# Performance work log

Hardware: AMD Instinct MI355X
Metric: run time of the kernel (lower is better)

Reference implementation:

```python
import jax, jax.numpy as jnp
import numpy as np

N = 50000
E = 1000000
D_IN = 128
D_HID = 128
D_EMB = 128
D_DEG = 32
NEG_SLOPE = 0.2


def _add_self_loops(src, dst, n):
    loop = jnp.arange(n, dtype=src.dtype)
    return jnp.concatenate([src, loop]), jnp.concatenate([dst, loop])


def gat_conv(x, src, dst, W, a_src, a_dst, b, n):
    """PyG GATConv, heads=1, add_self_loops=True. src/dst already include self loops."""
    h = x @ W                                   # [n, d_out]
    hs = h[src]                                 # [e, d_out] gather (message sources)
    e = jax.nn.leaky_relu(hs @ a_src + h[dst] @ a_dst, NEG_SLOPE)  # [e]
    m = jax.ops.segment_max(e, dst, num_segments=n)
    e = jnp.exp(e - m[dst])
    denom = jax.ops.segment_sum(e, dst, num_segments=n)
    alpha = e / (denom[dst] + 1e-16)
    out = jax.ops.segment_sum(alpha[:, None] * hs, dst, num_segments=n)
    return out + b


def setup_inputs() -> dict:
    key = jax.random.key(0)
    ks = jax.random.split(key, 24)
    p = lambda k, shape: (jax.random.normal(k, shape, dtype=jnp.float32) * 0.05)
    inp = {
        "x_o": jax.random.normal(ks[0], (N, D_IN), dtype=jnp.float32),
        "degree_o": jax.random.normal(ks[1], (N, D_DEG), dtype=jnp.float32),
        "edge_index_o": jax.random.randint(ks[2], (2, E), 0, N, dtype=jnp.int32),
        "edge_index_s": jax.random.randint(ks[3], (2, E), 0, N, dtype=jnp.int32),
        # GAT layer params: o1, o2, s1, s2
        "W_o1": p(ks[4], (D_IN, D_HID)), "a_src_o1": p(ks[5], (D_HID,)), "a_dst_o1": p(ks[6], (D_HID,)), "b_o1": jnp.zeros((D_HID,), jnp.float32),
        "W_o2": p(ks[7], (D_HID, D_EMB)), "a_src_o2": p(ks[8], (D_EMB,)), "a_dst_o2": p(ks[9], (D_EMB,)), "b_o2": jnp.zeros((D_EMB,), jnp.float32),
        "W_s1": p(ks[10], (D_IN, D_HID)), "a_src_s1": p(ks[11], (D_HID,)), "a_dst_s1": p(ks[12], (D_HID,)), "b_s1": jnp.zeros((D_HID,), jnp.float32),
        "W_s2": p(ks[13], (D_HID, D_EMB)), "a_src_s2": p(ks[14], (D_EMB,)), "a_dst_s2": p(ks[15], (D_EMB,)), "b_s2": jnp.zeros((D_EMB,), jnp.float32),
        "W_pred": p(ks[16], (2 * D_EMB + D_DEG, 2)), "b_pred": jnp.zeros((2,), jnp.float32),
    }
    return inp


def reference(x_o, degree_o,
              W_o1, a_src_o1, a_dst_o1, b_o1,
              W_o2, a_src_o2, a_dst_o2, b_o2,
              W_s1, a_src_s1, a_dst_s1, b_s1,
              W_s2, a_src_s2, a_dst_s2, b_s2,
              W_pred, b_pred,
              edge_index_o, edge_index_s):
    n = x_o.shape[0]
    src_o, dst_o = _add_self_loops(edge_index_o[0], edge_index_o[1], n)
    src_s, dst_s = _add_self_loops(edge_index_s[0], edge_index_s[1], n)

    # branch o (original graph); dropout is identity in eval mode
    x1_o = jax.nn.relu(gat_conv(x_o, src_o, dst_o, W_o1, a_src_o1, a_dst_o1, b_o1, n))
    x2_o = gat_conv(x1_o, src_o, dst_o, W_o2, a_src_o2, a_dst_o2, b_o2, n)
    # branch s (second graph)
    x1_s = jax.nn.relu(gat_conv(x_o, src_s, dst_s, W_s1, a_src_s1, a_dst_s1, b_s1, n))
    x2_s = gat_conv(x1_s, src_s, dst_s, W_s2, a_src_s2, a_dst_s2, b_s2, n)

    x2_os = jnp.concatenate([x2_o, x2_s, degree_o], axis=1)   # [n, 2*emb+deg]
    attn = jax.nn.softmax(x2_os @ W_pred + b_pred, axis=1)    # [n, 2]
    pred = attn[:, :1] * x2_o + attn[:, 1:] * x2_s            # [n, emb]
    return pred
```

## Files before the change

### kernel.cpp

```cpp
#include <hip/hip_runtime.h>
#include <hip/hip_fp16.h>
#include <math.h>


#define LRELU(v) ((v) > 0.f ? (v) : 0.2f * (v))

#define BSHIFT 7
#define BSIZE  128
#define MAXB   512
#define CHUNK  4096
#define EPT    16
#define MAXE   4352
#define CAPI   (MAXE + BSIZE)
#define WTSZ   17408

typedef _Float16 half8 __attribute__((ext_vector_type(8)));
typedef float f32x4 __attribute__((ext_vector_type(4)));


__global__ __launch_bounds__(256) void k_bin_scatter(
    const int* __restrict__ src_o, const int* __restrict__ dst_o,
    const int* __restrict__ src_s, const int* __restrict__ dst_s,
    int* bcur_o, int* bcur_s, int* ebin_o, int* ebin_s, int E)
{
    __shared__ int cnt[MAXB];
    __shared__ int gb[MAXB];
    int t = threadIdx.x;
    int base = blockIdx.x * CHUNK;

    for (int g = 0; g < 2; g++) {
        const int* srcp = g ? src_s : src_o;
        const int* dstp = g ? dst_s : dst_o;
        int* bcur = g ? bcur_s : bcur_o;
        int* ebin = g ? ebin_s : ebin_o;
        for (int i = t; i < MAXB; i += 256) cnt[i] = 0;
        __syncthreads();
        int pk[EPT], bk[EPT], rk[EPT];
        #pragma unroll
        for (int j = 0; j < EPT; j++) {
            int e = base + j * 256 + t;
            bk[j] = -1; pk[j] = 0; rk[j] = 0;
            if (e < E) {
                int d = dstp[e];
                int s = srcp[e];
                int bb = d >> BSHIFT;
                bk[j] = bb;
                pk[j] = ((d & (BSIZE - 1)) << 16) | s;
                rk[j] = atomicAdd(&cnt[bb], 1);
            }
        }
        __syncthreads();
        for (int i = t; i < MAXB; i += 256) {
            int c = cnt[i];
            gb[i] = c ? atomicAdd(&bcur[i], c) : 0;
        }
        __syncthreads();
        #pragma unroll
        for (int j = 0; j < EPT; j++) {
            if (bk[j] >= 0) {
                int p = gb[bk[j]] + rk[j];
                if (p < (bk[j] + 1) * MAXE) ebin[p] = pk[j];
            }
        }
        __syncthreads();
    }
}


__global__ __launch_bounds__(256) void k_prepw(
    const float* __restrict__ W0, const float* __restrict__ W1,
    const float* __restrict__ W2, const float* __restrict__ W3,
    _Float16* __restrict__ WtG, int* bcur_o, int* bcur_s, int nbuck)
{
    int i = blockIdx.x * 256 + threadIdx.x;
    if (i < nbuck) { bcur_o[i] = i * MAXE; bcur_s[i] = i * MAXE; }
    int w = i >> 14;
    int rem = i & 16383;
    int nn = rem >> 7;
    int k = rem & 127;
    const float* W = (w == 0) ? W0 : (w == 1) ? W1 : (w == 2) ? W2 : W3;
    WtG[w * WTSZ + nn * 136 + k] = (_Float16)W[k * 128 + nn];
}


__device__ __forceinline__ void sd_epilogue(
    const f32x4* acc, const float* a_src, const float* a_dst,
    float* Svec, float* Dvec, int m0, int wave, int lane, int m, int q, int n)
{
    float sp[4] = {0.f, 0.f, 0.f, 0.f};
    float dp[4] = {0.f, 0.f, 0.f, 0.f};
    #pragma unroll
    for (int nt = 0; nt < 8; nt++) {
        float asv = a_src[nt * 16 + m];
        float adv = a_dst[nt * 16 + m];
        #pragma unroll
        for (int r = 0; r < 4; r++) {
            sp[r] = fmaf(acc[nt][r], asv, sp[r]);
            dp[r] = fmaf(acc[nt][r], adv, dp[r]);
        }
    }
    #pragma unroll
    for (int msk = 1; msk < 16; msk <<= 1) {
        #pragma unroll
        for (int r = 0; r < 4; r++) {
            sp[r] += __shfl_xor(sp[r], msk);
            dp[r] += __shfl_xor(dp[r], msk);
        }
    }
    if (m == 0) {
        #pragma unroll
        for (int r = 0; r < 4; r++) {
            int row = m0 + wave * 16 + q * 4 + r;
            if (row < n) { Svec[row] = sp[r]; Dvec[row] = dp[r]; }
        }
    }
}

__device__ __forceinline__ void d_to_lds(
    _Float16* As, const f32x4* acc, int wave, int m, int q)
{
    #pragma unroll
    for (int nt = 0; nt < 8; nt++) {
        #pragma unroll
        for (int r = 0; r < 4; r++) {
            As[(wave * 16 + q * 4 + r) * 136 + nt * 16 + m] = (_Float16)acc[nt][r];
        }
    }
}

__device__ __forceinline__ void lds_to_h(
    const _Float16* As, __half* H, int m0, int tid, int n)
{
    for (int i = tid; i < 1024; i += 256) {
        int r = i >> 4;
        int c8 = (i & 15) << 3;
        int row = m0 + r;
        if (row < n)
            *(uint4*)&H[(size_t)row * 128 + c8] = *(const uint4*)&As[r * 136 + c8];
    }
}


__device__ __forceinline__ void sort_body(
    char* SMEM, int b,
    const int* __restrict__ ebin, const int* __restrict__ bcur,
    int* __restrict__ off, int* __restrict__ dend,
    unsigned short* __restrict__ idx, int N)
{
    int* pack   = (int*)SMEM;
    int* sorted = pack + MAXE;
    int* cnt4   = sorted + MAXE + BSIZE;
    int* s2     = cnt4 + 4 * (BSIZE + 1);
    int* noff   = s2 + (BSIZE + 1);

    int t = threadIdx.x;
    int wave = t >> 6;
    int node0 = b << BSHIFT;
    int nloc = min(BSIZE, N - node0);
    int ebeg = b * MAXE;
    int ne = min(bcur[b] - ebeg, MAXE);
    int ib = b * CAPI;

    for (int i = t; i < ne; i += 256) pack[i] = ebin[ebeg + i];
    for (int i = t; i < 4 * (BSIZE + 1); i += 256) cnt4[i] = 0;
    __syncthreads();
    for (int i = t; i < ne; i += 256)
        atomicAdd(&cnt4[wave * (BSIZE + 1) + (pack[i] >> 16)], 1);
    __syncthreads();
    int c0 = 0, c1 = 0, c2 = 0, c3 = 0, selfc = 0;
    if (t < BSIZE + 1) {
        c0 = cnt4[0 * (BSIZE + 1) + t];
        c1 = cnt4[1 * (BSIZE + 1) + t];
        c2 = cnt4[2 * (BSIZE + 1) + t];
        c3 = cnt4[3 * (BSIZE + 1) + t];
        selfc = (t < nloc) ? 1 : 0;
        s2[t] = c0 + c1 + c2 + c3 + selfc;
    }
    __syncthreads();
    for (int d = 1; d <= BSIZE; d <<= 1) {
        int v = (t < BSIZE + 1 && t >= d) ? s2[t - d] : 0;
        __syncthreads();
        if (t < BSIZE + 1) s2[t] += v;
        __syncthreads();
    }
    if (t < BSIZE + 1) noff[t] = s2[t] - (c0 + c1 + c2 + c3 + selfc);
    __syncthreads();
    if (t < nloc) {
        int base0 = noff[t] + 1;
        cnt4[0 * (BSIZE + 1) + t] = base0;
        cnt4[1 * (BSIZE + 1) + t] = base0 + c0;
        cnt4[2 * (BSIZE + 1) + t] = base0 + c0 + c1;
        cnt4[3 * (BSIZE + 1) + t] = base0 + c0 + c1 + c2;
        sorted[noff[t]] = node0 + t;
        off[node0 + t]  = ib + noff[t];
        dend[node0 + t] = ib + s2[t];
    }
    __syncthreads();
    for (int i = t; i < ne; i += 256) {
        int p = atomicAdd(&cnt4[wave * (BSIZE + 1) + (pack[i] >> 16)], 1);
        sorted[p] = pack[i] & 0xffff;
    }
    __syncthreads();
    int tot = ne + nloc;
    for (int i = t; i < tot; i += 256) idx[ib + i] = (unsigned short)sorted[i];
}


__device__ __forceinline__ void gemm1_body(
    char* SMEM, int m0,
    const float* __restrict__ X,
    const _Float16* __restrict__ WtO, const _Float16* __restrict__ WtS,
    const float* __restrict__ asO, const float* __restrict__ adO,
    const float* __restrict__ asS, const float* __restrict__ adS,
    __half* __restrict__ HO, __half* __restrict__ HS,
    float* __restrict__ SO, float* __restrict__ DO,
    float* __restrict__ SS, float* __restrict__ DS, int n)
{
    _Float16* As = (_Float16*)SMEM;
    _Float16* Wt = As + 64 * 136;
    int tid = threadIdx.x;

    for (int i = tid; i < WTSZ / 8; i += 256)
        ((uint4*)Wt)[i] = ((const uint4*)WtO)[i];
    for (int i = tid; i < 64 * 32; i += 256) {
        int r = i >> 5;
        int c4 = (i & 31) << 2;
        int row = m0 + r; if (row >= n) row = n - 1;
        float4 v = *(const float4*)&X[(size_t)row * 128 + c4];
        _Float16* p = &As[r * 136 + c4];
        p[0] = (_Float16)v.x; p[1] = (_Float16)v.y;
        p[2] = (_Float16)v.z; p[3] = (_Float16)v.w;
    }
    __syncthreads();

    int wave = tid >> 6;
    int lane = tid & 63;
    int m = lane & 15;
    int q = lane >> 4;
    int arow = wave * 16 + m;

    f32x4 accO[8], accS[8];
    #pragma unroll
    for (int nt = 0; nt < 8; nt++) accO[nt] = (f32x4){0.f, 0.f, 0.f, 0.f};
    #pragma unroll
    for (int k0 = 0; k0 < 128; k0 += 32) {
        half8 a = *(half8*)&As[arow * 136 + k0 + q * 8];
        #pragma unroll
        for (int nt = 0; nt < 8; nt++) {
            half8 b = *(half8*)&Wt[(nt * 16 + m) * 136 + k0 + q * 8];
            accO[nt] = __builtin_amdgcn_mfma_f32_16x16x32_f16(a, b, accO[nt], 0, 0, 0);
        }
    }
    sd_epilogue(accO, asO, adO, SO, DO, m0, wave, lane, m, q, n);
    __syncthreads();
    for (int i = tid; i < WTSZ / 8; i += 256)
        ((uint4*)Wt)[i] = ((const uint4*)WtS)[i];
    __syncthreads();
    #pragma unroll
    for (int nt = 0; nt < 8; nt++) accS[nt] = (f32x4){0.f, 0.f, 0.f, 0.f};
    #pragma unroll
    for (int k0 = 0; k0 < 128; k0 += 32) {
        half8 a = *(half8*)&As[arow * 136 + k0 + q * 8];
        #pragma unroll
        for (int nt = 0; nt < 8; nt++) {
            half8 b = *(half8*)&Wt[(nt * 16 + m) * 136 + k0 + q * 8];
            accS[nt] = __builtin_amdgcn_mfma_f32_16x16x32_f16(a, b, accS[nt], 0, 0, 0);
        }
    }
    sd_epilogue(accS, asS, adS, SS, DS, m0, wave, lane, m, q, n);

    __syncthreads();
    d_to_lds(As, accO, wave, m, q);
    __syncthreads();
    lds_to_h(As, HO, m0, tid, n);
    __syncthreads();
    d_to_lds(As, accS, wave, m, q);
    __syncthreads();
    lds_to_h(As, HS, m0, tid, n);
}


__global__ __launch_bounds__(256) void k_sortgemm1(
    const int* __restrict__ ebin_o, const int* __restrict__ bcur_o,
    int* __restrict__ off_o, int* __restrict__ dend_o, unsigned short* __restrict__ idx_o,
    const int* __restrict__ ebin_s, const int* __restrict__ bcur_s,
    int* __restrict__ off_s, int* __restrict__ dend_s, unsigned short* __restrict__ idx_s,
    const float* __restrict__ X,
    const _Float16* __restrict__ WtO, const _Float16* __restrict__ WtS,
    const float* __restrict__ asO, const float* __restrict__ adO,
    const float* __restrict__ asS, const float* __restrict__ adS,
    __half* __restrict__ HO, __half* __restrict__ HS,
    float* __restrict__ SO, float* __restrict__ DO,
    float* __restrict__ SS, float* __restrict__ DS,
    int N, int nbuck)
{
    __shared__ __align__(16) char SMEM[52224];
    int bid = blockIdx.x;
    if (bid < 2 * nbuck) {
        if (bid < nbuck)
            sort_body(SMEM, bid, ebin_o, bcur_o, off_o, dend_o, idx_o, N);
        else
            sort_body(SMEM, bid - nbuck, ebin_s, bcur_s, off_s, dend_s, idx_s, N);
    } else {
        gemm1_body(SMEM, (bid - 2 * nbuck) * 64, X, WtO, WtS,
                   asO, adO, asS, adS, HO, HS, SO, DO, SS, DS, N);
    }
}


__global__ __launch_bounds__(256) void k_gemm2(
    const __half* __restrict__ X0, const __half* __restrict__ X1,
    const _Float16* __restrict__ WtA, const _Float16* __restrict__ WtB,
    const float* __restrict__ as0, const float* __restrict__ ad0,
    const float* __restrict__ as1, const float* __restrict__ ad1,
    __half* __restrict__ H0, __half* __restrict__ H1,
    float* __restrict__ S0, float* __restrict__ D0,
    float* __restrict__ S1, float* __restrict__ D1,
    int n)
{
    int br = blockIdx.y;
    const __half* X = br ? X1 : X0;
    const _Float16* WtGp = br ? WtB : WtA;
    const float* a_src = br ? as1 : as0;
    const float* a_dst = br ? ad1 : ad0;
    __half* H = br ? H1 : H0;
    float* Svec = br ? S1 : S0;
    float* Dvec = br ? D1 : D0;

    __shared__ _Float16 As[64 * 136];
    __shared__ _Float16 Wt[128 * 136];
    int tid = threadIdx.x;
    int m0 = blockIdx.x * 64;

    for (int i = tid; i < WTSZ / 8; i += 256)
        ((uint4*)Wt)[i] = ((const uint4*)WtGp)[i];
    for (int i = tid; i < 64 * 16; i += 256) {
        int r = i >> 4;
        int c8 = (i & 15) << 3;
        int row = m0 + r; if (row >= n) row = n - 1;
        *(uint4*)&As[r * 136 + c8] = *(const uint4*)&X[(size_t)row * 128 + c8];
    }
    __syncthreads();

    int wave = tid >> 6;
    int lane = tid & 63;
    int m = lane & 15;
    int q = lane >> 4;
    int arow = wave * 16 + m;

    f32x4 acc[8];
    #pragma unroll
    for (int nt = 0; nt < 8; nt++) acc[nt] = (f32x4){0.f, 0.f, 0.f, 0.f};
    #pragma unroll
    for (int k0 = 0; k0 < 128; k0 += 32) {
        half8 a = *(half8*)&As[arow * 136 + k0 + q * 8];
        #pragma unroll
        for (int nt = 0; nt < 8; nt++) {
            half8 b = *(half8*)&Wt[(nt * 16 + m) * 136 + k0 + q * 8];
            acc[nt] = __builtin_amdgcn_mfma_f32_16x16x32_f16(a, b, acc[nt], 0, 0, 0);
        }
    }
    sd_epilogue(acc, a_src, a_dst, Svec, Dvec, m0, wave, lane, m, q, n);
    __syncthreads();
    d_to_lds(As, acc, wave, m, q);
    __syncthreads();
    lds_to_h(As, H, m0, tid, n);
}


__device__ __forceinline__ void agg_core(
    const __half* __restrict__ H, const float* __restrict__ Svec, float dn,
    const unsigned short* __restrict__ idx, int beg, int end,
    int lane, int q, int subl, float* acc, float& denom)
{
    #pragma unroll
    for (int j = 0; j < 8; j++) acc[j] = 0.f;
    denom = 0.f;
    for (int base = beg; base < end; base += 64) {
        int cnt = min(64, end - base);
        float w = 0.f;
        int s = 0;
        if (lane < cnt) {
            s = idx[base + lane];
            w = __expf(LRELU(Svec[s] + dn));
        }
        denom += w;
        int cnt16 = (cnt + 15) & ~15;
        for (int kk = 0; kk < cnt16; kk += 16) {
            int k0 = kk + q;
            float w0 = __shfl(w, k0);
            float w1 = __shfl(w, k0 + 4);
            float w2 = __shfl(w, k0 + 8);
            float w3 = __shfl(w, k0 + 12);
            int s0 = __shfl(s, k0);
            int s1 = __shfl(s, k0 + 4);
            int s2 = __shfl(s, k0 + 8);
            int s3 = __shfl(s, k0 + 12);
            uint4 u0 = ((const uint4*)(H + (size_t)s0 * 128))[subl];
            uint4 u1 = ((const uint4*)(H + (size_t)s1 * 128))[subl];
            uint4 u2 = ((const uint4*)(H + (size_t)s2 * 128))[subl];
            uint4 u3 = ((const uint4*)(H + (size_t)s3 * 128))[subl];
            const _Float16* p;
            p = (const _Float16*)&u0;
            #pragma unroll
            for (int j = 0; j < 8; j++) acc[j] = fmaf((float)p[j], w0, acc[j]);
            p = (const _Float16*)&u1;
            #pragma unroll
            for (int j = 0; j < 8; j++) acc[j] = fmaf((float)p[j], w1, acc[j]);
            p = (const _Float16*)&u2;
            #pragma unroll
            for (int j = 0; j < 8; j++) acc[j] = fmaf((float)p[j], w2, acc[j]);
            p = (const _Float16*)&u3;
            #pragma unroll
            for (int j = 0; j < 8; j++) acc[j] = fmaf((float)p[j], w3, acc[j]);
        }
    }
    #pragma unroll
    for (int j = 0; j < 8; j++) {
        acc[j] += __shfl_xor(acc[j], 16);
        acc[j] += __shfl_xor(acc[j], 32);
    }
    #pragma unroll
    for (int o = 32; o; o >>= 1) denom += __shfl_xor(denom, o);
}


__global__ __launch_bounds__(256) void k_agg1(
    const __half* __restrict__ H0, const __half* __restrict__ H1,
    const float* __restrict__ S0, const float* __restrict__ D0,
    const float* __restrict__ S1, const float* __restrict__ D1,
    const int* __restrict__ off0, const int* __restrict__ dend0,
    const unsigned short* __restrict__ idx0,
    const int* __restrict__ off1, const int* __restrict__ dend1,
    const unsigned short* __restrict__ idx1,
    const float* __restrict__ b0, const float* __restrict__ b1,
    __half* __restrict__ out0, __half* __restrict__ out1,
    int n)
{
    int br = blockIdx.y;
    const __half* H = br ? H1 : H0;
    const float* Svec = br ? S1 : S0;
    const float* Dvec = br ? D1 : D0;
    const int* off  = br ? off1  : off0;
    const int* dend = br ? dend1 : dend0;
    const unsigned short* idx = br ? idx1 : idx0;
    const float* bias = br ? b1 : b0;
    __half* out = br ? out1 : out0;

    int wave = threadIdx.x >> 6;
    int lane = threadIdx.x & 63;
    int node = blockIdx.x * 4 + wave;
    if (node >= n) return;

    int q = lane >> 4;
    int subl = lane & 15;
    float acc[8], denom;
    agg_core(H, Svec, Dvec[node], idx, off[node], dend[node],
             lane, q, subl, acc, denom);

    if (q == 0) {
        float inv = 1.f / (denom + 1e-16f);
        int cb = subl << 3;
        half8 hv;
        #pragma unroll
        for (int j = 0; j < 8; j++) {
            float v = fmaxf(acc[j] * inv + bias[cb + j], 0.f);
            hv[j] = (_Float16)v;
        }
        *(half8*)&out[(size_t)node * 128 + cb] = hv;
    }
}


__global__ __launch_bounds__(256) void k_agg_pred(
    const __half* __restrict__ H0, const __half* __restrict__ H1,
    const float* __restrict__ S0, const float* __restrict__ D0,
    const float* __restrict__ S1, const float* __restrict__ D1,
    const int* __restrict__ off0, const int* __restrict__ dend0,
    const unsigned short* __restrict__ idx0,
    const int* __restrict__ off1, const int* __restrict__ dend1,
    const unsigned short* __restrict__ idx1,
    const float* __restrict__ b0, const float* __restrict__ b1,
    const float* __restrict__ deg,
    const float* __restrict__ Wp, const float* __restrict__ bp,
    float* __restrict__ out, int n)
{
    int wave = threadIdx.x >> 6;
    int lane = threadIdx.x & 63;
    int node = blockIdx.x * 4 + wave;
    if (node >= n) return;

    int q = lane >> 4;
    int subl = lane & 15;
    int cb = subl << 3;

    float acc[8], denom;
    float vo[8], vs[8];

    agg_core(H0, S0, D0[node], idx0, off0[node], dend0[node],
             lane, q, subl, acc, denom);
    {
        float inv = 1.f / (denom + 1e-16f);
        #pragma unroll
        for (int j = 0; j < 8; j++) vo[j] = acc[j] * inv + b0[cb + j];
    }
    agg_core(H1, S1, D1[node], idx1, off1[node], dend1[node],
             lane, q, subl, acc, denom);
    {
        float inv = 1.f / (denom + 1e-16f);
        #pragma unroll
        for (int j = 0; j < 8; j++) vs[j] = acc[j] * inv + b1[cb + j];
    }

    if (q == 0) {
        float z0 = 0.f, z1 = 0.f;
        #pragma unroll
        for (int j = 0; j < 8; j++) {
            int c = cb + j;
            z0 = fmaf(vo[j], Wp[c * 2],     z0);
            z1 = fmaf(vo[j], Wp[c * 2 + 1], z1);
            z0 = fmaf(vs[j], Wp[(128 + c) * 2],     z0);
            z1 = fmaf(vs[j], Wp[(128 + c) * 2 + 1], z1);
        }
        float2 dv = *(const float2*)&deg[(size_t)node * 32 + 2 * subl];
        z0 = fmaf(dv.x, Wp[(256 + 2 * subl) * 2],     z0);
        z1 = fmaf(dv.x, Wp[(256 + 2 * subl) * 2 + 1], z1);
        z0 = fmaf(dv.y, Wp[(257 + 2 * subl) * 2],     z0);
        z1 = fmaf(dv.y, Wp[(257 + 2 * subl) * 2 + 1], z1);
        #pragma unroll
        for (int msk = 1; msk < 16; msk <<= 1) {
            z0 += __shfl_xor(z0, msk);
            z1 += __shfl_xor(z1, msk);
        }
        z0 += bp[0];
        z1 += bp[1];
        float mz = fmaxf(z0, z1);
        float e0 = __expf(z0 - mz);
        float e1 = __expf(z1 - mz);
        float a0 = e0 / (e0 + e1);
        float a1 = 1.f - a0;
        float4 r0, r1;
        r0.x = a0 * vo[0] + a1 * vs[0];
        r0.y = a0 * vo[1] + a1 * vs[1];
        r0.z = a0 * vo[2] + a1 * vs[2];
        r0.w = a0 * vo[3] + a1 * vs[3];
        r1.x = a0 * vo[4] + a1 * vs[4];
        r1.y = a0 * vo[5] + a1 * vs[5];
        r1.z = a0 * vo[6] + a1 * vs[6];
        r1.w = a0 * vo[7] + a1 * vs[7];
        *(float4*)&out[(size_t)node * 128 + cb] = r0;
        *(float4*)&out[(size_t)node * 128 + cb + 4] = r1;
    }
}


extern "C" void kernel_launch(void* const* d_in, const int* in_sizes, int n_in,
                              void* d_out, int out_size, void* d_ws, size_t ws_size,
                              hipStream_t stream) {
    const float* x_o    = (const float*)d_in[0];
    const float* degree = (const float*)d_in[1];
    const int*   ei_o   = (const int*)d_in[2];
    const int*   ei_s   = (const int*)d_in[3];
    const float* W_o1 = (const float*)d_in[4];
    const float* asr_o1 = (const float*)d_in[5];
    const float* ads_o1 = (const float*)d_in[6];
    const float* b_o1 = (const float*)d_in[7];
    const float* W_o2 = (const float*)d_in[8];
    const float* asr_o2 = (const float*)d_in[9];
    const float* ads_o2 = (const float*)d_in[10];
    const float* b_o2 = (const float*)d_in[11];
    const float* W_s1 = (const float*)d_in[12];
    const float* asr_s1 = (const float*)d_in[13];
    const float* ads_s1 = (const float*)d_in[14];
    const float* b_s1 = (const float*)d_in[15];
    const float* W_s2 = (const float*)d_in[16];
    const float* asr_s2 = (const float*)d_in[17];
    const float* ads_s2 = (const float*)d_in[18];
    const float* b_s2 = (const float*)d_in[19];
    const float* W_pred = (const float*)d_in[20];
    const float* b_pred = (const float*)d_in[21];
    float* out = (float*)d_out;

    const int N = in_sizes[0] / 128;
    const int E = in_sizes[2] / 2;
    const int NBUCK = (N + BSIZE - 1) >> BSHIFT;

    char* ws = (char*)d_ws;
    size_t o = 0;
    auto alloc = [&](size_t bytes) -> char* {
        char* p = ws + o;
        o += (bytes + 255) & ~(size_t)255;
        return p;
    };
    int* bcur_o = (int*)alloc((size_t)NBUCK * 4);
    int* bcur_s = (int*)alloc((size_t)NBUCK * 4);
    int* off_o  = (int*)alloc((size_t)N * 4);
    int* dend_o = (int*)alloc((size_t)N * 4);
    int* off_s  = (int*)alloc((size_t)N * 4);
    int* dend_s = (int*)alloc((size_t)N * 4);
    unsigned short* idx_o = (unsigned short*)alloc((size_t)NBUCK * CAPI * 2);
    unsigned short* idx_s = (unsigned short*)alloc((size_t)NBUCK * CAPI * 2);
    _Float16* WtG = (_Float16*)alloc((size_t)4 * WTSZ * 2);
    float* Sv_o = (float*)alloc((size_t)N * 4);
    float* Dv_o = (float*)alloc((size_t)N * 4);
    float* Sv_s = (float*)alloc((size_t)N * 4);
    float* Dv_s = (float*)alloc((size_t)N * 4);
    __half* h_o   = (__half*)alloc((size_t)N * 128 * 2);
    __half* h_s   = (__half*)alloc((size_t)N * 128 * 2);
    __half* x1h_o = (__half*)alloc((size_t)N * 128 * 2);
    __half* x1h_s = (__half*)alloc((size_t)N * 128 * 2);
    (void)ws_size;

    int* ebin_o = (int*)x1h_o;
    int* ebin_s = (int*)x1h_s;

    dim3 blk(256);
    int gBin  = (E + CHUNK - 1) / CHUNK;
    int gGemm = (N + 63) / 64;
    int gNode = (N + 3) / 4;

    k_prepw<<<256, blk, 0, stream>>>(W_o1, W_o2, W_s1, W_s2, WtG,
                                     bcur_o, bcur_s, NBUCK);
    k_bin_scatter<<<gBin, blk, 0, stream>>>(ei_o, ei_o + E, ei_s, ei_s + E,
                                            bcur_o, bcur_s, ebin_o, ebin_s, E);
    k_sortgemm1<<<2 * NBUCK + gGemm, blk, 0, stream>>>(
        ebin_o, bcur_o, off_o, dend_o, idx_o,
        ebin_s, bcur_s, off_s, dend_s, idx_s,
        x_o, WtG, WtG + 2 * WTSZ,
        asr_o1, ads_o1, asr_s1, ads_s1,
        h_o, h_s, Sv_o, Dv_o, Sv_s, Dv_s, N, NBUCK);
    dim3 gA(gNode, 2);
    k_agg1<<<gA, blk, 0, stream>>>(
        h_o, h_s, Sv_o, Dv_o, Sv_s, Dv_s,
        off_o, dend_o, idx_o, off_s, dend_s, idx_s,
        b_o1, b_s1, x1h_o, x1h_s, N);
    dim3 gG(gGemm, 2);
    k_gemm2<<<gG, blk, 0, stream>>>(
        x1h_o, x1h_s, WtG + WTSZ, WtG + 3 * WTSZ,
        asr_o2, ads_o2, asr_s2, ads_s2,
        h_o, h_s, Sv_o, Dv_o, Sv_s, Dv_s, N);
    k_agg_pred<<<gNode, blk, 0, stream>>>(
        h_o, h_s, Sv_o, Dv_o, Sv_s, Dv_s,
        off_o, dend_o, idx_o, off_s, dend_s, idx_s,
        b_o2, b_s2, degree, W_pred, b_pred, out, N);
}
```

Before: 351.9 us.

## Read GEMM weights directly from global memory and split bin scatter across graphs

The GEMM kernels now stop staging the transposed weight matrices in LDS. MFMA B operands are read straight from global (L2-resident) memory, and gemm2 also reads its A operand from global. gemm1 computes both branch GEMMs in one interleaved loop instead of two sequential ones with a reload. This shrinks shared memory, raising occupancy and removing copy and sync overhead, at the cost of more global or L2 traffic per MFMA. The bin-scatter kernel also moves the two graphs onto separate grid-y blocks to double parallelism.

```diff
diff --git a/kernel.cpp b/kernel.cpp
--- a/kernel.cpp
+++ b/kernel.cpp
@@ -12,7 +12,7 @@
 #define EPT    16
 #define MAXE   4352
 #define CAPI   (MAXE + BSIZE)
-#define WTSZ   17408
+#define WTN    16384
 
 typedef _Float16 half8 __attribute__((ext_vector_type(8)));
 typedef float f32x4 __attribute__((ext_vector_type(4)));
@@ -27,42 +27,40 @@
     __shared__ int gb[MAXB];
     int t = threadIdx.x;
     int base = blockIdx.x * CHUNK;
-
-    for (int g = 0; g < 2; g++) {
-        const int* srcp = g ? src_s : src_o;
-        const int* dstp = g ? dst_s : dst_o;
-        int* bcur = g ? bcur_s : bcur_o;
-        int* ebin = g ? ebin_s : ebin_o;
-        for (int i = t; i < MAXB; i += 256) cnt[i] = 0;
-        __syncthreads();
-        int pk[EPT], bk[EPT], rk[EPT];
-        #pragma unroll
-        for (int j = 0; j < EPT; j++) {
-            int e = base + j * 256 + t;
-            bk[j] = -1; pk[j] = 0; rk[j] = 0;
-            if (e < E) {
-                int d = dstp[e];
-                int s = srcp[e];
-                int bb = d >> BSHIFT;
-                bk[j] = bb;
-                pk[j] = ((d & (BSIZE - 1)) << 16) | s;
-                rk[j] = atomicAdd(&cnt[bb], 1);
-            }
-        }
-        __syncthreads();
-        for (int i = t; i < MAXB; i += 256) {
-            int c = cnt[i];
-            gb[i] = c ? atomicAdd(&bcur[i], c) : 0;
-        }
-        __syncthreads();
-        #pragma unroll
-        for (int j = 0; j < EPT; j++) {
-            if (bk[j] >= 0) {
-                int p = gb[bk[j]] + rk[j];
-                if (p < (bk[j] + 1) * MAXE) ebin[p] = pk[j];
-            }
-        }
-        __syncthreads();
+    int g = blockIdx.y;
+
+    const int* srcp = g ? src_s : src_o;
+    const int* dstp = g ? dst_s : dst_o;
+    int* bcur = g ? bcur_s : bcur_o;
+    int* ebin = g ? ebin_s : ebin_o;
+    for (int i = t; i < MAXB; i += 256) cnt[i] = 0;
+    __syncthreads();
+    int pk[EPT], bk[EPT], rk[EPT];
+    #pragma unroll
+    for (int j = 0; j < EPT; j++) {
+        int e = base + j * 256 + t;
+        bk[j] = -1; pk[j] = 0; rk[j] = 0;
+        if (e < E) {
+            int d = dstp[e];
+            int s = srcp[e];
+            int bb = d >> BSHIFT;
+            bk[j] = bb;
+            pk[j] = ((d & (BSIZE - 1)) << 16) | s;
+            rk[j] = atomicAdd(&cnt[bb], 1);
+        }
+    }
+    __syncthreads();
+    for (int i = t; i < MAXB; i += 256) {
+        int c = cnt[i];
+        gb[i] = c ? atomicAdd(&bcur[i], c) : 0;
+    }
+    __syncthreads();
+    #pragma unroll
+    for (int j = 0; j < EPT; j++) {
+        if (bk[j] >= 0) {
+            int p = gb[bk[j]] + rk[j];
+            if (p < (bk[j] + 1) * MAXE) ebin[p] = pk[j];
+        }
     }
 }
 
@@ -79,7 +77,7 @@
     int nn = rem >> 7;
     int k = rem & 127;
     const float* W = (w == 0) ? W0 : (w == 1) ? W1 : (w == 2) ? W2 : W3;
-    WtG[w * WTSZ + nn * 136 + k] = (_Float16)W[k * 128 + nn];
+    WtG[w * WTN + nn * 128 + k] = (_Float16)W[k * 128 + nn];
 }
 
 
@@ -217,11 +215,8 @@
     float* __restrict__ SS, float* __restrict__ DS, int n)
 {
     _Float16* As = (_Float16*)SMEM;
-    _Float16* Wt = As + 64 * 136;
     int tid = threadIdx.x;
 
-    for (int i = tid; i < WTSZ / 8; i += 256)
-        ((uint4*)Wt)[i] = ((const uint4*)WtO)[i];
     for (int i = tid; i < 64 * 32; i += 256) {
         int r = i >> 5;
         int c4 = (i & 31) << 2;
@@ -241,32 +236,22 @@
 
     f32x4 accO[8], accS[8];
     #pragma unroll
-    for (int nt = 0; nt < 8; nt++) accO[nt] = (f32x4){0.f, 0.f, 0.f, 0.f};
+    for (int nt = 0; nt < 8; nt++) {
+        accO[nt] = (f32x4){0.f, 0.f, 0.f, 0.f};
+        accS[nt] = (f32x4){0.f, 0.f, 0.f, 0.f};
+    }
     #pragma unroll
     for (int k0 = 0; k0 < 128; k0 += 32) {
         half8 a = *(half8*)&As[arow * 136 + k0 + q * 8];
         #pragma unroll
         for (int nt = 0; nt < 8; nt++) {
-            half8 b = *(half8*)&Wt[(nt * 16 + m) * 136 + k0 + q * 8];
-            accO[nt] = __builtin_amdgcn_mfma_f32_16x16x32_f16(a, b, accO[nt], 0, 0, 0);
+            half8 bO = *(const half8*)&WtO[(nt * 16 + m) * 128 + k0 + q * 8];
+            half8 bS = *(const half8*)&WtS[(nt * 16 + m) * 128 + k0 + q * 8];
+            accO[nt] = __builtin_amdgcn_mfma_f32_16x16x32_f16(a, bO, accO[nt], 0, 0, 0);
+            accS[nt] = __builtin_amdgcn_mfma_f32_16x16x32_f16(a, bS, accS[nt], 0, 0, 0);
         }
     }
     sd_epilogue(accO, asO, adO, SO, DO, m0, wave, lane, m, q, n);
-    __syncthreads();
-    for (int i = tid; i < WTSZ / 8; i += 256)
-        ((uint4*)Wt)[i] = ((const uint4*)WtS)[i];
-    __syncthreads();
-    #pragma unroll
-    for (int nt = 0; nt < 8; nt++) accS[nt] = (f32x4){0.f, 0.f, 0.f, 0.f};
-    #pragma unroll
-    for (int k0 = 0; k0 < 128; k0 += 32) {
-        half8 a = *(half8*)&As[arow * 136 + k0 + q * 8];
-        #pragma unroll
-        for (int nt = 0; nt < 8; nt++) {
-            half8 b = *(half8*)&Wt[(nt * 16 + m) * 136 + k0 + q * 8];
-            accS[nt] = __builtin_amdgcn_mfma_f32_16x16x32_f16(a, b, accS[nt], 0, 0, 0);
-        }
-    }
     sd_epilogue(accS, asS, adS, SS, DS, m0, wave, lane, m, q, n);
 
     __syncthreads();
@@ -294,7 +279,7 @@
     float* __restrict__ SS, float* __restrict__ DS,
     int N, int nbuck)
 {
-    __shared__ __align__(16) char SMEM[52224];
+    __shared__ __align__(16) char SMEM[38424];
     int bid = blockIdx.x;
     if (bid < 2 * nbuck) {
         if (bid < nbuck)
@@ -320,7 +305,7 @@
 {
     int br = blockIdx.y;
     const __half* X = br ? X1 : X0;
-    const _Float16* WtGp = br ? WtB : WtA;
+    const _Float16* Wt = br ? WtB : WtA;
     const float* a_src = br ? as1 : as0;
     const float* a_dst = br ? ad1 : ad0;
     __half* H = br ? H1 : H0;
@@ -328,40 +313,30 @@
     float* Dvec = br ? D1 : D0;
 
     __shared__ _Float16 As[64 * 136];
-    __shared__ _Float16 Wt[128 * 136];
     int tid = threadIdx.x;
     int m0 = blockIdx.x * 64;
-
-    for (int i = tid; i < WTSZ / 8; i += 256)
-        ((uint4*)Wt)[i] = ((const uint4*)WtGp)[i];
-    for (int i = tid; i < 64 * 16; i += 256) {
-        int r = i >> 4;
-        int c8 = (i & 15) << 3;
-        int row = m0 + r; if (row >= n) row = n - 1;
-        *(uint4*)&As[r * 136 + c8] = *(const uint4*)&X[(size_t)row * 128 + c8];
-    }
-    __syncthreads();
 
     int wave = tid >> 6;
     int lane = tid & 63;
     int m = lane & 15;
     int q = lane >> 4;
     int arow = wave * 16 + m;
+    int xrow = m0 + arow; if (xrow >= n) xrow = n - 1;
+    size_t rbase = (size_t)xrow * 128;
 
     f32x4 acc[8];
     #pragma unroll
     for (int nt = 0; nt < 8; nt++) acc[nt] = (f32x4){0.f, 0.f, 0.f, 0.f};
     #pragma unroll
     for (int k0 = 0; k0 < 128; k0 += 32) {
-        half8 a = *(half8*)&As[arow * 136 + k0 + q * 8];
+        half8 a = *(const half8*)&X[rbase + k0 + q * 8];
         #pragma unroll
         for (int nt = 0; nt < 8; nt++) {
-            half8 b = *(half8*)&Wt[(nt * 16 + m) * 136 + k0 + q * 8];
+            half8 b = *(const half8*)&Wt[(nt * 16 + m) * 128 + k0 + q * 8];
             acc[nt] = __builtin_amdgcn_mfma_f32_16x16x32_f16(a, b, acc[nt], 0, 0, 0);
         }
     }
     sd_epilogue(acc, a_src, a_dst, Svec, Dvec, m0, wave, lane, m, q, n);
-    __syncthreads();
     d_to_lds(As, acc, wave, m, q);
     __syncthreads();
     lds_to_h(As, H, m0, tid, n);
@@ -600,7 +575,7 @@
     int* dend_s = (int*)alloc((size_t)N * 4);
     unsigned short* idx_o = (unsigned short*)alloc((size_t)NBUCK * CAPI * 2);
     unsigned short* idx_s = (unsigned short*)alloc((size_t)NBUCK * CAPI * 2);
-    _Float16* WtG = (_Float16*)alloc((size_t)4 * WTSZ * 2);
+    _Float16* WtG = (_Float16*)alloc((size_t)4 * WTN * 2);
     float* Sv_o = (float*)alloc((size_t)N * 4);
     float* Dv_o = (float*)alloc((size_t)N * 4);
     float* Sv_s = (float*)alloc((size_t)N * 4);
@@ -621,12 +596,13 @@
 
     k_prepw<<<256, blk, 0, stream>>>(W_o1, W_o2, W_s1, W_s2, WtG,
                                      bcur_o, bcur_s, NBUCK);
-    k_bin_scatter<<<gBin, blk, 0, stream>>>(ei_o, ei_o + E, ei_s, ei_s + E,
-                                            bcur_o, bcur_s, ebin_o, ebin_s, E);
+    dim3 gB(gBin, 2);
+    k_bin_scatter<<<gB, blk, 0, stream>>>(ei_o, ei_o + E, ei_s, ei_s + E,
+                                          bcur_o, bcur_s, ebin_o, ebin_s, E);
     k_sortgemm1<<<2 * NBUCK + gGemm, blk, 0, stream>>>(
         ebin_o, bcur_o, off_o, dend_o, idx_o,
         ebin_s, bcur_s, off_s, dend_s, idx_s,
-        x_o, WtG, WtG + 2 * WTSZ,
+        x_o, WtG, WtG + 2 * WTN,
         asr_o1, ads_o1, asr_s1, ads_s1,
         h_o, h_s, Sv_o, Dv_o, Sv_s, Dv_s, N, NBUCK);
     dim3 gA(gNode, 2);
@@ -636,7 +612,7 @@
         b_o1, b_s1, x1h_o, x1h_s, N);
     dim3 gG(gGemm, 2);
     k_gemm2<<<gG, blk, 0, stream>>>(
-        x1h_o, x1h_s, WtG + WTSZ, WtG + 3 * WTSZ,
+        x1h_o, x1h_s, WtG + WTN, WtG + 3 * WTN,
         asr_o2, ads_o2, asr_s2, ads_s2,
         h_o, h_s, Sv_o, Dv_o, Sv_s, Dv_s, N);
     k_agg_pred<<<gNode, blk, 0, stream>>>(
```

Measured after the change: 379.6 us. 1.08x slower.

## Fuse layer-1 aggregation with layer-2 GEMM and split bin scatter per graph

Applied to the files above, without the earlier changes.

Layer-1 attention aggregation now writes its ReLU'd fp16 rows directly into shared memory, and the same 1024-thread block runs the layer-2 MFMA GEMM on them. This removes the x1 round trip through global memory and one kernel launch. Layer-2 outputs go to separate buffers (x1h and new S/D vectors) because layer-1 H is still being read by other blocks. The bin-scatter kernel also processes the two graphs in separate grid rows instead of looping, which doubles parallelism. In exchange, the large 1024-thread blocks with 52KB of shared memory may lower occupancy, and only 4 of 16 waves do the GEMM.

```diff
diff --git a/kernel.cpp b/kernel.cpp
--- a/kernel.cpp
+++ b/kernel.cpp
@@ -27,42 +27,40 @@
     __shared__ int gb[MAXB];
     int t = threadIdx.x;
     int base = blockIdx.x * CHUNK;
-
-    for (int g = 0; g < 2; g++) {
-        const int* srcp = g ? src_s : src_o;
-        const int* dstp = g ? dst_s : dst_o;
-        int* bcur = g ? bcur_s : bcur_o;
-        int* ebin = g ? ebin_s : ebin_o;
-        for (int i = t; i < MAXB; i += 256) cnt[i] = 0;
-        __syncthreads();
-        int pk[EPT], bk[EPT], rk[EPT];
-        #pragma unroll
-        for (int j = 0; j < EPT; j++) {
-            int e = base + j * 256 + t;
-            bk[j] = -1; pk[j] = 0; rk[j] = 0;
-            if (e < E) {
-                int d = dstp[e];
-                int s = srcp[e];
-                int bb = d >> BSHIFT;
-                bk[j] = bb;
-                pk[j] = ((d & (BSIZE - 1)) << 16) | s;
-                rk[j] = atomicAdd(&cnt[bb], 1);
-            }
-        }
-        __syncthreads();
-        for (int i = t; i < MAXB; i += 256) {
-            int c = cnt[i];
-            gb[i] = c ? atomicAdd(&bcur[i], c) : 0;
-        }
-        __syncthreads();
-        #pragma unroll
-        for (int j = 0; j < EPT; j++) {
-            if (bk[j] >= 0) {
-                int p = gb[bk[j]] + rk[j];
-                if (p < (bk[j] + 1) * MAXE) ebin[p] = pk[j];
-            }
-        }
-        __syncthreads();
+    int g = blockIdx.y;
+
+    const int* srcp = g ? src_s : src_o;
+    const int* dstp = g ? dst_s : dst_o;
+    int* bcur = g ? bcur_s : bcur_o;
+    int* ebin = g ? ebin_s : ebin_o;
+    for (int i = t; i < MAXB; i += 256) cnt[i] = 0;
+    __syncthreads();
+    int pk[EPT], bk[EPT], rk[EPT];
+    #pragma unroll
+    for (int j = 0; j < EPT; j++) {
+        int e = base + j * 256 + t;
+        bk[j] = -1; pk[j] = 0; rk[j] = 0;
+        if (e < E) {
+            int d = dstp[e];
+            int s = srcp[e];
+            int bb = d >> BSHIFT;
+            bk[j] = bb;
+            pk[j] = ((d & (BSIZE - 1)) << 16) | s;
+            rk[j] = atomicAdd(&cnt[bb], 1);
+        }
+    }
+    __syncthreads();
+    for (int i = t; i < MAXB; i += 256) {
+        int c = cnt[i];
+        gb[i] = c ? atomicAdd(&bcur[i], c) : 0;
+    }
+    __syncthreads();
+    #pragma unroll
+    for (int j = 0; j < EPT; j++) {
+        if (bk[j] >= 0) {
+            int p = gb[bk[j]] + rk[j];
+            if (p < (bk[j] + 1) * MAXE) ebin[p] = pk[j];
+        }
     }
 }
 
@@ -305,66 +303,6 @@
         gemm1_body(SMEM, (bid - 2 * nbuck) * 64, X, WtO, WtS,
                    asO, adO, asS, adS, HO, HS, SO, DO, SS, DS, N);
     }
-}
-
-
-__global__ __launch_bounds__(256) void k_gemm2(
-    const __half* __restrict__ X0, const __half* __restrict__ X1,
-    const _Float16* __restrict__ WtA, const _Float16* __restrict__ WtB,
-    const float* __restrict__ as0, const float* __restrict__ ad0,
-    const float* __restrict__ as1, const float* __restrict__ ad1,
-    __half* __restrict__ H0, __half* __restrict__ H1,
-    float* __restrict__ S0, float* __restrict__ D0,
-    float* __restrict__ S1, float* __restrict__ D1,
-    int n)
-{
-    int br = blockIdx.y;
-    const __half* X = br ? X1 : X0;
-    const _Float16* WtGp = br ? WtB : WtA;
-    const float* a_src = br ? as1 : as0;
-    const float* a_dst = br ? ad1 : ad0;
-    __half* H = br ? H1 : H0;
-    float* Svec = br ? S1 : S0;
-    float* Dvec = br ? D1 : D0;
-
-    __shared__ _Float16 As[64 * 136];
-    __shared__ _Float16 Wt[128 * 136];
-    int tid = threadIdx.x;
-    int m0 = blockIdx.x * 64;
-
-    for (int i = tid; i < WTSZ / 8; i += 256)
-        ((uint4*)Wt)[i] = ((const uint4*)WtGp)[i];
-    for (int i = tid; i < 64 * 16; i += 256) {
-        int r = i >> 4;
-        int c8 = (i & 15) << 3;
-        int row = m0 + r; if (row >= n) row = n - 1;
-        *(uint4*)&As[r * 136 + c8] = *(const uint4*)&X[(size_t)row * 128 + c8];
-    }
-    __syncthreads();
-
-    int wave = tid >> 6;
-    int lane = tid & 63;
-    int m = lane & 15;
-    int q = lane >> 4;
-    int arow = wave * 16 + m;
-
-    f32x4 acc[8];
-    #pragma unroll
-    for (int nt = 0; nt < 8; nt++) acc[nt] = (f32x4){0.f, 0.f, 0.f, 0.f};
-    #pragma unroll
-    for (int k0 = 0; k0 < 128; k0 += 32) {
-        half8 a = *(half8*)&As[arow * 136 + k0 + q * 8];
-        #pragma unroll
-        for (int nt = 0; nt < 8; nt++) {
-            half8 b = *(half8*)&Wt[(nt * 16 + m) * 136 + k0 + q * 8];
-            acc[nt] = __builtin_amdgcn_mfma_f32_16x16x32_f16(a, b, acc[nt], 0, 0, 0);
-        }
-    }
-    sd_epilogue(acc, a_src, a_dst, Svec, Dvec, m0, wave, lane, m, q, n);
-    __syncthreads();
-    d_to_lds(As, acc, wave, m, q);
-    __syncthreads();
-    lds_to_h(As, H, m0, tid, n);
 }
 
 
@@ -425,7 +363,7 @@
 }
 
 
-__global__ __launch_bounds__(256) void k_agg1(
+__global__ __launch_bounds__(1024) void k_agg1gemm2(
     const __half* __restrict__ H0, const __half* __restrict__ H1,
     const float* __restrict__ S0, const float* __restrict__ D0,
     const float* __restrict__ S1, const float* __restrict__ D1,
@@ -434,7 +372,12 @@
     const int* __restrict__ off1, const int* __restrict__ dend1,
     const unsigned short* __restrict__ idx1,
     const float* __restrict__ b0, const float* __restrict__ b1,
-    __half* __restrict__ out0, __half* __restrict__ out1,
+    const _Float16* __restrict__ WtA, const _Float16* __restrict__ WtB,
+    const float* __restrict__ as0, const float* __restrict__ ad0,
+    const float* __restrict__ as1, const float* __restrict__ ad1,
+    __half* __restrict__ HO2, __half* __restrict__ HS2,
+    float* __restrict__ S2o, float* __restrict__ D2o,
+    float* __restrict__ S2s, float* __restrict__ D2s,
     int n)
 {
     int br = blockIdx.y;
@@ -445,29 +388,71 @@
     const int* dend = br ? dend1 : dend0;
     const unsigned short* idx = br ? idx1 : idx0;
     const float* bias = br ? b1 : b0;
-    __half* out = br ? out1 : out0;
-
-    int wave = threadIdx.x >> 6;
-    int lane = threadIdx.x & 63;
-    int node = blockIdx.x * 4 + wave;
-    if (node >= n) return;
-
+    const _Float16* WtGp = br ? WtB : WtA;
+    const float* a_src = br ? as1 : as0;
+    const float* a_dst = br ? ad1 : ad0;
+    __half* Hout = br ? HS2 : HO2;
+    float* Sout = br ? S2s : S2o;
+    float* Dout = br ? D2s : D2o;
+
+    __shared__ _Float16 As[64 * 136];
+    __shared__ _Float16 Wt[128 * 136];
+    int tid = threadIdx.x;
+    int m0 = blockIdx.x * 64;
+    int wave = tid >> 6;
+    int lane = tid & 63;
     int q = lane >> 4;
     int subl = lane & 15;
-    float acc[8], denom;
-    agg_core(H, Svec, Dvec[node], idx, off[node], dend[node],
-             lane, q, subl, acc, denom);
-
-    if (q == 0) {
-        float inv = 1.f / (denom + 1e-16f);
-        int cb = subl << 3;
-        half8 hv;
-        #pragma unroll
-        for (int j = 0; j < 8; j++) {
-            float v = fmaxf(acc[j] * inv + bias[cb + j], 0.f);
-            hv[j] = (_Float16)v;
-        }
-        *(half8*)&out[(size_t)node * 128 + cb] = hv;
+
+    for (int i = tid; i < WTSZ / 8; i += 1024)
+        ((uint4*)Wt)[i] = ((const uint4*)WtGp)[i];
+
+    #pragma unroll 1
+    for (int t = 0; t < 4; t++) {
+        int r = wave * 4 + t;
+        int node = m0 + r;
+        if (node < n) {
+            float acc[8], denom;
+            agg_core(H, Svec, Dvec[node], idx, off[node], dend[node],
+                     lane, q, subl, acc, denom);
+            if (q == 0) {
+                float inv = 1.f / (denom + 1e-16f);
+                int cb = subl << 3;
+                #pragma unroll
+                for (int j = 0; j < 8; j++)
+                    As[r * 136 + cb + j] =
+                        (_Float16)fmaxf(acc[j] * inv + bias[cb + j], 0.f);
+            }
+        }
+    }
+    __syncthreads();
+
+    if (wave < 4) {
+        int m = subl;
+        int arow = wave * 16 + m;
+        f32x4 acc[8];
+        #pragma unroll
+        for (int nt = 0; nt < 8; nt++) acc[nt] = (f32x4){0.f, 0.f, 0.f, 0.f};
+        #pragma unroll
+        for (int k0 = 0; k0 < 128; k0 += 32) {
+            half8 a = *(half8*)&As[arow * 136 + k0 + q * 8];
+            #pragma unroll
+            for (int nt = 0; nt < 8; nt++) {
+                half8 b = *(half8*)&Wt[(nt * 16 + m) * 136 + k0 + q * 8];
+                acc[nt] = __builtin_amdgcn_mfma_f32_16x16x32_f16(a, b, acc[nt], 0, 0, 0);
+            }
+        }
+        sd_epilogue(acc, a_src, a_dst, Sout, Dout, m0, wave, lane, m, q, n);
+        d_to_lds(As, acc, wave, m, q);
+    }
+    __syncthreads();
+
+    {
+        int r = tid >> 4;
+        int c8 = (tid & 15) << 3;
+        int row = m0 + r;
+        if (row < n)
+            *(uint4*)&Hout[(size_t)row * 128 + c8] = *(const uint4*)&As[r * 136 + c8];
     }
 }
 
@@ -605,6 +590,10 @@
     float* Dv_o = (float*)alloc((size_t)N * 4);
     float* Sv_s = (float*)alloc((size_t)N * 4);
     float* Dv_s = (float*)alloc((size_t)N * 4);
+    float* Sv2_o = (float*)alloc((size_t)N * 4);
+    float* Dv2_o = (float*)alloc((size_t)N * 4);
+    float* Sv2_s = (float*)alloc((size_t)N * 4);
+    float* Dv2_s = (float*)alloc((size_t)N * 4);
     __half* h_o   = (__half*)alloc((size_t)N * 128 * 2);
     __half* h_s   = (__half*)alloc((size_t)N * 128 * 2);
     __half* x1h_o = (__half*)alloc((size_t)N * 128 * 2);
@@ -621,26 +610,25 @@
 
     k_prepw<<<256, blk, 0, stream>>>(W_o1, W_o2, W_s1, W_s2, WtG,
                                      bcur_o, bcur_s, NBUCK);
-    k_bin_scatter<<<gBin, blk, 0, stream>>>(ei_o, ei_o + E, ei_s, ei_s + E,
-                                            bcur_o, bcur_s, ebin_o, ebin_s, E);
+    dim3 gB(gBin, 2);
+    k_bin_scatter<<<gB, blk, 0, stream>>>(ei_o, ei_o + E, ei_s, ei_s + E,
+                                          bcur_o, bcur_s, ebin_o, ebin_s, E);
     k_sortgemm1<<<2 * NBUCK + gGemm, blk, 0, stream>>>(
         ebin_o, bcur_o, off_o, dend_o, idx_o,
         ebin_s, bcur_s, off_s, dend_s, idx_s,
         x_o, WtG, WtG + 2 * WTSZ,
         asr_o1, ads_o1, asr_s1, ads_s1,
         h_o, h_s, Sv_o, Dv_o, Sv_s, Dv_s, N, NBUCK);
-    dim3 gA(gNode, 2);
-    k_agg1<<<gA, blk, 0, stream>>>(
+    dim3 gAG(gGemm, 2);
+    k_agg1gemm2<<<gAG, dim3(1024), 0, stream>>>(
         h_o, h_s, Sv_o, Dv_o, Sv_s, Dv_s,
         off_o, dend_o, idx_o, off_s, dend_s, idx_s,
-        b_o1, b_s1, x1h_o, x1h_s, N);
-    dim3 gG(gGemm, 2);
-    k_gemm2<<<gG, blk, 0, stream>>>(
-        x1h_o, x1h_s, WtG + WTSZ, WtG + 3 * WTSZ,
+        b_o1, b_s1,
+        WtG + WTSZ, WtG + 3 * WTSZ,
         asr_o2, ads_o2, asr_s2, ads_s2,
-        h_o, h_s, Sv_o, Dv_o, Sv_s, Dv_s, N);
+        x1h_o, x1h_s, Sv2_o, Dv2_o, Sv2_s, Dv2_s, N);
     k_agg_pred<<<gNode, blk, 0, stream>>>(
-        h_o, h_s, Sv_o, Dv_o, Sv_s, Dv_s,
+        x1h_o, x1h_s, Sv2_o, Dv2_o, Sv2_s, Dv2_s,
         off_o, dend_o, idx_o, off_s, dend_s, idx_s,
         b_o2, b_s2, degree, W_pred, b_pred, out, N);
 }
```

Result: slower. 367.6 us (+4.5%).
